# Optimization experiments

Measured on AMD Instinct MI355X. Metric: run time of the kernel, lower is better.

Reference implementation:

```python
import jax, jax.numpy as jnp
import numpy as np

NOISE_STD = 0.05
ALPHA = 0.2
RHO = 1.0
B, T, I, H, O = 128, 1000, 4, 512, 2

def setup_inputs() -> dict:
    key = jax.random.key(0)
    k_in, k_no, k_wi, k_wr, k_wo = jax.random.split(key, 5)
    return {
        "input": jax.random.normal(k_in, (B, T, I), dtype=jnp.float32),
        "noise": jax.random.normal(k_no, (B, T, H), dtype=jnp.float32),
        "wi": jax.random.normal(k_wi, (I, H), dtype=jnp.float32),
        "si": jnp.ones((I,), dtype=jnp.float32),
        "wrec": jax.random.normal(k_wr, (H, H), dtype=jnp.float32) * (RHO / np.sqrt(H)),
        "wo": jax.random.normal(k_wo, (H, O), dtype=jnp.float32) * (1.0 / np.sqrt(H)),
        "so": jnp.ones((O,), dtype=jnp.float32),
        "h0": jnp.zeros((H,), dtype=jnp.float32),
    }

def reference(input, noise, wi, si, wrec, wo, so, h0):
    # wi_full = (wi.T * si).T == wi * si[:, None]; wo_full = wo * so
    wi_full = wi * si[:, None]            # [I, H]
    wo_full = wo * so                     # [H, O]
    # pre-project inputs for all timesteps in one GEMM: [B, T, H]
    inp_proj = jnp.einsum('bti,ih->bth', input, wi_full)
    drive = NOISE_STD * noise + ALPHA * inp_proj  # fused per-step additive term
    h_init = jnp.broadcast_to(h0, (B, H))

    def step(h, d_t):
        r = jnp.tanh(h)
        h_new = h + d_t + ALPHA * (-h + r @ wrec.T)
        r_new = jnp.tanh(h_new)
        return h_new, r_new @ wo_full

    # scan over time: drive transposed to [T, B, H]
    _, out = jax.lax.scan(step, h_init, jnp.swapaxes(drive, 0, 1))
    return jnp.swapaxes(out, 0, 1)        # [B, T, O]
```

## Files before the change

### kernel.cpp

```cpp
#include <hip/hip_runtime.h>
#include <math.h>


#define Bn 128
#define Tn 1000
#define In 4
#define Hn 512
#define On 2
#define ALPHA 0.2f
#define NSTD 0.05f

#define KC 72
#define KR 128
#define KS (Hn - KC - KR)

__global__ void prep_kernel(const float* __restrict__ wi, const float* __restrict__ si,
                            const float* __restrict__ wrec, const float* __restrict__ wo,
                            const float* __restrict__ so,
                            float* __restrict__ wrecT, float* __restrict__ wi_full,
                            float* __restrict__ wo_full) {
    int idx = blockIdx.x * blockDim.x + threadIdx.x;
    int stride = gridDim.x * blockDim.x;
    for (int e = idx; e < Hn * Hn; e += stride) {
        int j = e & (Hn - 1);
        int k = e >> 9;
        wrecT[k * Hn + j] = wrec[j * Hn + k];
    }
    if (idx < In * Hn) wi_full[idx] = wi[idx] * si[idx >> 9];
    if (idx < Hn * On) wo_full[idx] = wo[idx] * so[idx & 1];
}

__global__ __launch_bounds__(512) void rnn_kernel(
    const float* __restrict__ input, const float* __restrict__ noise,
    const float* __restrict__ h0, const float* __restrict__ wrecT,
    const float* __restrict__ wi_full, const float* __restrict__ wo_full,
    float* __restrict__ out) {
    extern __shared__ float lds[];
    float* wlds = lds;
    float* r_s  = lds + KC * Hn;
    float* red  = r_s + Hn;

    const int j = threadIdx.x;
    const int b = blockIdx.x;

    for (int k = 0; k < KC; ++k)
        wlds[k * Hn + j] = wrecT[k * Hn + j];

    float wreg[KR];
#pragma unroll
    for (int k = 0; k < KR; ++k)
        wreg[k] = wrecT[(KC + k) * Hn + j];

    const float wi0 = wi_full[j],          wi1 = wi_full[Hn + j],
                wi2 = wi_full[2 * Hn + j], wi3 = wi_full[3 * Hn + j];
    const float wo0 = wo_full[j * On], wo1 = wo_full[j * On + 1];

    float h = h0[j];
    r_s[j] = tanhf(h);
    __syncthreads();

    const float* __restrict__ noise_p = noise + (size_t)b * Tn * Hn + j;
    const float* __restrict__ inp_p   = input + (size_t)b * Tn * In;
    float*       __restrict__ out_p   = out   + (size_t)b * Tn * On;
    const float* __restrict__ wstr    = wrecT + (size_t)(KC + KR) * Hn + j;

    const int lane = j & 63;
    const int wid  = j >> 6;
    const float4* r4 = (const float4*)r_s;

    for (int t = 0; t < Tn; ++t) {
        float  nz  = noise_p[(size_t)t * Hn];
        float4 inp = *(const float4*)(inp_p + t * In);

        float a0 = 0.f, a1 = 0.f, a2 = 0.f, a3 = 0.f;

#pragma unroll 6
        for (int g = 0; g < KC / 4; ++g) {
            float4 rv = r4[g];
            const float* wp = wlds + 4 * g * Hn + j;
            a0 = fmaf(rv.x, wp[0],      a0);
            a1 = fmaf(rv.y, wp[Hn],     a1);
            a2 = fmaf(rv.z, wp[2 * Hn], a2);
            a3 = fmaf(rv.w, wp[3 * Hn], a3);
        }
#pragma unroll
        for (int g = 0; g < KR / 4; ++g) {
            float4 rv = r4[KC / 4 + g];
            a0 = fmaf(rv.x, wreg[4 * g + 0], a0);
            a1 = fmaf(rv.y, wreg[4 * g + 1], a1);
            a2 = fmaf(rv.z, wreg[4 * g + 2], a2);
            a3 = fmaf(rv.w, wreg[4 * g + 3], a3);
        }
#pragma unroll 4
        for (int g = 0; g < KS / 4; ++g) {
            float4 rv = r4[(KC + KR) / 4 + g];
            const float* wp = wstr + (size_t)4 * g * Hn;
            a0 = fmaf(rv.x, wp[0],      a0);
            a1 = fmaf(rv.y, wp[Hn],     a1);
            a2 = fmaf(rv.z, wp[2 * Hn], a2);
            a3 = fmaf(rv.w, wp[3 * Hn], a3);
        }
        float acc = (a0 + a1) + (a2 + a3);

        float drive = NSTD * nz +
                      ALPHA * (inp.x * wi0 + inp.y * wi1 + inp.z * wi2 + inp.w * wi3);
        h = h + drive + ALPHA * (acc - h);
        float rn = tanhf(h);

        float p0 = rn * wo0, p1 = rn * wo1;
#pragma unroll
        for (int off = 32; off > 0; off >>= 1) {
            p0 += __shfl_down(p0, off, 64);
            p1 += __shfl_down(p1, off, 64);
        }

        __syncthreads();
        r_s[j] = rn;
        if (lane == 0) { red[wid * 2] = p0; red[wid * 2 + 1] = p1; }
        __syncthreads();
        if (j == 0) {
            float s0 = 0.f, s1 = 0.f;
#pragma unroll
            for (int w = 0; w < 8; ++w) { s0 += red[2 * w]; s1 += red[2 * w + 1]; }
            out_p[t * On]     = s0;
            out_p[t * On + 1] = s1;
        }
    }
}

extern "C" void kernel_launch(void* const* d_in, const int* in_sizes, int n_in,
                              void* d_out, int out_size, void* d_ws, size_t ws_size,
                              hipStream_t stream) {
    const float* input = (const float*)d_in[0];
    const float* noise = (const float*)d_in[1];
    const float* wi    = (const float*)d_in[2];
    const float* si    = (const float*)d_in[3];
    const float* wrec  = (const float*)d_in[4];
    const float* wo    = (const float*)d_in[5];
    const float* so    = (const float*)d_in[6];
    const float* h0    = (const float*)d_in[7];
    float* out = (float*)d_out;

    float* wrecT   = (float*)d_ws;
    float* wi_full = wrecT + Hn * Hn;
    float* wo_full = wi_full + In * Hn;

    prep_kernel<<<512, 512, 0, stream>>>(wi, si, wrec, wo, so, wrecT, wi_full, wo_full);

    const size_t lds_bytes = (size_t)(KC * Hn + Hn + 16) * sizeof(float);
    hipFuncSetAttribute((const void*)rnn_kernel,
                        hipFuncAttributeMaxDynamicSharedMemorySize, (int)lds_bytes);
    rnn_kernel<<<Bn, Hn, lds_bytes, stream>>>(input, noise, h0, wrecT, wi_full,
                                              wo_full, out);
}
```

Baseline: 9.673 ms.

## Split each batch row across two workgroups exchanging hidden state via global flags

Each batch element is now handled by two 512-thread workgroups, each owning half of the hidden units. Within a workgroup the two 256-thread halves split the K dimension. The halves of a pair trade their new tanh activations each step through a double-buffered global buffer with acquire/release flag spinning, and add output partial sums atomically. This puts the whole recurrent weight matrix in LDS and registers rather than streaming part of it from global memory, and doubles the number of CUs in use. The cost is a cross-workgroup spin-wait every timestep, which relies on both workgroups of a pair being resident at once and adds latency on the serial critical path.

```diff
diff --git a/kernel.cpp b/kernel.cpp
--- a/kernel.cpp
+++ b/kernel.cpp
@@ -10,15 +10,16 @@
 #define ALPHA 0.2f
 #define NSTD 0.05f
 
-#define KC 72
-#define KR 128
-#define KS (Hn - KC - KR)
+#define HALF 256
+#define LR 72
+#define RR 92
 
 __global__ void prep_kernel(const float* __restrict__ wi, const float* __restrict__ si,
                             const float* __restrict__ wrec, const float* __restrict__ wo,
                             const float* __restrict__ so,
                             float* __restrict__ wrecT, float* __restrict__ wi_full,
-                            float* __restrict__ wo_full) {
+                            float* __restrict__ wo_full, float* __restrict__ out,
+                            int* __restrict__ flags) {
     int idx = blockIdx.x * blockDim.x + threadIdx.x;
     int stride = gridDim.x * blockDim.x;
     for (int e = idx; e < Hn * Hn; e += stride) {
@@ -28,102 +29,171 @@
     }
     if (idx < In * Hn) wi_full[idx] = wi[idx] * si[idx >> 9];
     if (idx < Hn * On) wo_full[idx] = wo[idx] * so[idx & 1];
+    for (int e = idx; e < Bn * Tn * On; e += stride) out[e] = 0.f;
+    if (idx < Bn * 2) flags[idx] = 0;
 }
 
-__global__ __launch_bounds__(512) void rnn_kernel(
+__global__ __launch_bounds__(512, 2) void rnn_kernel(
     const float* __restrict__ input, const float* __restrict__ noise,
     const float* __restrict__ h0, const float* __restrict__ wrecT,
     const float* __restrict__ wi_full, const float* __restrict__ wo_full,
-    float* __restrict__ out) {
+    float* xbuf, int* flags, float* __restrict__ out) {
     extern __shared__ float lds[];
-    float* wlds = lds;
-    float* r_s  = lds + KC * Hn;
-    float* red  = r_s + Hn;
-
-    const int j = threadIdx.x;
-    const int b = blockIdx.x;
-
-    for (int k = 0; k < KC; ++k)
-        wlds[k * Hn + j] = wrecT[k * Hn + j];
-
-    float wreg[KR];
-#pragma unroll
-    for (int k = 0; k < KR; ++k)
-        wreg[k] = wrecT[(KC + k) * Hn + j];
-
-    const float wi0 = wi_full[j],          wi1 = wi_full[Hn + j],
-                wi2 = wi_full[2 * Hn + j], wi3 = wi_full[3 * Hn + j];
-    const float wo0 = wo_full[j * On], wo1 = wo_full[j * On + 1];
-
-    float h = h0[j];
-    r_s[j] = tanhf(h);
+    float* wl0  = lds;
+    float* wl1  = lds + LR * HALF;
+    float* r_s  = lds + 2 * LR * HALF;
+    float* pacc = r_s + Hn;
+    float* red  = pacc + HALF;
+
+    const int tid  = threadIdx.x;
+    const int c    = tid & (HALF - 1);
+    const int hh   = tid >> 8;
+
+    const int bid  = blockIdx.x;
+    const int g    = bid & 7;
+    const int s    = bid >> 3;
+    const int b    = g * 16 + (s >> 1);
+    const int half = s & 1;
+
+    const int base0 = half * HALF;
+    const int base1 = (1 - half) * HALF;
+    const int gc    = half * HALF + c;
+
+    for (int e = tid; e < LR * HALF; e += 512) {
+        int lr = e >> 8;
+        int cc = e & 255;
+        int dst = (lr >> 2) * 1024 + cc * 4 + (lr & 3);
+        wl0[dst] = wrecT[(base0 + lr) * Hn + half * HALF + cc];
+        wl1[dst] = wrecT[(base1 + lr) * Hn + half * HALF + cc];
+    }
+
+    float w0[RR], w1[RR];
+#pragma unroll
+    for (int i = 0; i < RR; ++i)
+        w0[i] = wrecT[(base0 + LR + hh * RR + i) * Hn + gc];
+#pragma unroll
+    for (int i = 0; i < RR; ++i)
+        w1[i] = wrecT[(base1 + LR + hh * RR + i) * Hn + gc];
+#pragma unroll
+    for (int i = 0; i < RR; ++i) asm volatile("" : "+v"(w0[i]));
+#pragma unroll
+    for (int i = 0; i < RR; ++i) asm volatile("" : "+v"(w1[i]));
+
+    const float wi0 = wi_full[0 * Hn + gc], wi1 = wi_full[1 * Hn + gc],
+                wi2 = wi_full[2 * Hn + gc], wi3 = wi_full[3 * Hn + gc];
+    const float wo0 = wo_full[gc * On + 0], wo1 = wo_full[gc * On + 1];
+
+    float h = h0[gc];
+    r_s[tid] = tanhf(h0[tid]);
     __syncthreads();
 
-    const float* __restrict__ noise_p = noise + (size_t)b * Tn * Hn + j;
-    const float* __restrict__ inp_p   = input + (size_t)b * Tn * In;
-    float*       __restrict__ out_p   = out   + (size_t)b * Tn * On;
-    const float* __restrict__ wstr    = wrecT + (size_t)(KC + KR) * Hn + j;
-
-    const int lane = j & 63;
-    const int wid  = j >> 6;
-    const float4* r4 = (const float4*)r_s;
+    const float* noise_p = noise + (size_t)b * Tn * Hn + half * HALF + c;
+    const float* inp_p   = input + (size_t)b * Tn * In;
+    float*       out_p   = out   + (size_t)b * Tn * On;
+
+    float*       xb_mine = xbuf + (size_t)((b * 2 + half) * 2) * HALF;
+    const float* xb_part = xbuf + (size_t)((b * 2 + (1 - half)) * 2) * HALF;
+    int* flag_mine    = flags + b * 2 + half;
+    int* flag_partner = flags + b * 2 + (1 - half);
+
+    const float4* r4    = (const float4*)r_s;
+    const float4* wl4_0 = (const float4*)wl0;
+    const float4* wl4_1 = (const float4*)wl1;
+    const int rB0 = base0 >> 2, rB1 = base1 >> 2;
 
     for (int t = 0; t < Tn; ++t) {
-        float  nz  = noise_p[(size_t)t * Hn];
-        float4 inp = *(const float4*)(inp_p + t * In);
+        float nz = 0.f;
+        float4 inp = {0.f, 0.f, 0.f, 0.f};
+        if (hh == 0) {
+            nz  = noise_p[(size_t)t * Hn];
+            inp = *(const float4*)(inp_p + t * In);
+        }
 
         float a0 = 0.f, a1 = 0.f, a2 = 0.f, a3 = 0.f;
 
-#pragma unroll 6
-        for (int g = 0; g < KC / 4; ++g) {
-            float4 rv = r4[g];
-            const float* wp = wlds + 4 * g * Hn + j;
-            a0 = fmaf(rv.x, wp[0],      a0);
-            a1 = fmaf(rv.y, wp[Hn],     a1);
-            a2 = fmaf(rv.z, wp[2 * Hn], a2);
-            a3 = fmaf(rv.w, wp[3 * Hn], a3);
-        }
-#pragma unroll
-        for (int g = 0; g < KR / 4; ++g) {
-            float4 rv = r4[KC / 4 + g];
-            a0 = fmaf(rv.x, wreg[4 * g + 0], a0);
-            a1 = fmaf(rv.y, wreg[4 * g + 1], a1);
-            a2 = fmaf(rv.z, wreg[4 * g + 2], a2);
-            a3 = fmaf(rv.w, wreg[4 * g + 3], a3);
-        }
-#pragma unroll 4
-        for (int g = 0; g < KS / 4; ++g) {
-            float4 rv = r4[(KC + KR) / 4 + g];
-            const float* wp = wstr + (size_t)4 * g * Hn;
-            a0 = fmaf(rv.x, wp[0],      a0);
-            a1 = fmaf(rv.y, wp[Hn],     a1);
-            a2 = fmaf(rv.z, wp[2 * Hn], a2);
-            a3 = fmaf(rv.w, wp[3 * Hn], a3);
-        }
+#pragma unroll
+        for (int m = 0; m < LR / 8; ++m) {
+            float4 wv = wl4_0[(hh * 9 + m) * 256 + c];
+            float4 rv = r4[rB0 + hh * 9 + m];
+            a0 = fmaf(rv.x, wv.x, a0);
+            a1 = fmaf(rv.y, wv.y, a1);
+            a2 = fmaf(rv.z, wv.z, a2);
+            a3 = fmaf(rv.w, wv.w, a3);
+        }
+#pragma unroll
+        for (int m = 0; m < RR / 4; ++m) {
+            float4 rv = r4[rB0 + (LR >> 2) + hh * (RR >> 2) + m];
+            a0 = fmaf(rv.x, w0[4 * m + 0], a0);
+            a1 = fmaf(rv.y, w0[4 * m + 1], a1);
+            a2 = fmaf(rv.z, w0[4 * m + 2], a2);
+            a3 = fmaf(rv.w, w0[4 * m + 3], a3);
+        }
+
+        if (t > 0) {
+            if (tid == 0) {
+                while (__hip_atomic_load(flag_partner, __ATOMIC_ACQUIRE,
+                                         __HIP_MEMORY_SCOPE_AGENT) < t) {
+                    __builtin_amdgcn_s_sleep(1);
+                }
+            }
+            __syncthreads();
+            if (tid < HALF)
+                r_s[base1 + tid] = __hip_atomic_load(
+                    &xb_part[(t & 1) * HALF + tid], __ATOMIC_RELAXED,
+                    __HIP_MEMORY_SCOPE_AGENT);
+            __syncthreads();
+        }
+
+#pragma unroll
+        for (int m = 0; m < LR / 8; ++m) {
+            float4 wv = wl4_1[(hh * 9 + m) * 256 + c];
+            float4 rv = r4[rB1 + hh * 9 + m];
+            a0 = fmaf(rv.x, wv.x, a0);
+            a1 = fmaf(rv.y, wv.y, a1);
+            a2 = fmaf(rv.z, wv.z, a2);
+            a3 = fmaf(rv.w, wv.w, a3);
+        }
+#pragma unroll
+        for (int m = 0; m < RR / 4; ++m) {
+            float4 rv = r4[rB1 + (LR >> 2) + hh * (RR >> 2) + m];
+            a0 = fmaf(rv.x, w1[4 * m + 0], a0);
+            a1 = fmaf(rv.y, w1[4 * m + 1], a1);
+            a2 = fmaf(rv.z, w1[4 * m + 2], a2);
+            a3 = fmaf(rv.w, w1[4 * m + 3], a3);
+        }
+
         float acc = (a0 + a1) + (a2 + a3);
-
-        float drive = NSTD * nz +
-                      ALPHA * (inp.x * wi0 + inp.y * wi1 + inp.z * wi2 + inp.w * wi3);
-        h = h + drive + ALPHA * (acc - h);
-        float rn = tanhf(h);
-
-        float p0 = rn * wo0, p1 = rn * wo1;
-#pragma unroll
-        for (int off = 32; off > 0; off >>= 1) {
-            p0 += __shfl_down(p0, off, 64);
-            p1 += __shfl_down(p1, off, 64);
-        }
-
+        if (hh == 1) pacc[c] = acc;
         __syncthreads();
-        r_s[j] = rn;
-        if (lane == 0) { red[wid * 2] = p0; red[wid * 2 + 1] = p1; }
+        if (hh == 0) {
+            float total = acc + pacc[c];
+            float drive = NSTD * nz +
+                          ALPHA * (inp.x * wi0 + inp.y * wi1 +
+                                   inp.z * wi2 + inp.w * wi3);
+            h = h + drive + ALPHA * (total - h);
+            float rn = tanhf(h);
+            r_s[base0 + c] = rn;
+            xb_mine[((t + 1) & 1) * HALF + c] = rn;
+            float p0 = rn * wo0, p1 = rn * wo1;
+#pragma unroll
+            for (int off = 32; off > 0; off >>= 1) {
+                p0 += __shfl_down(p0, off, 64);
+                p1 += __shfl_down(p1, off, 64);
+            }
+            if ((tid & 63) == 0) {
+                red[(tid >> 6) * 2 + 0] = p0;
+                red[(tid >> 6) * 2 + 1] = p1;
+            }
+        }
         __syncthreads();
-        if (j == 0) {
-            float s0 = 0.f, s1 = 0.f;
-#pragma unroll
-            for (int w = 0; w < 8; ++w) { s0 += red[2 * w]; s1 += red[2 * w + 1]; }
-            out_p[t * On]     = s0;
-            out_p[t * On + 1] = s1;
+        if (tid == 0) {
+            __threadfence();
+            __hip_atomic_store(flag_mine, t + 1, __ATOMIC_RELEASE,
+                               __HIP_MEMORY_SCOPE_AGENT);
+            float s0 = red[0] + red[2] + red[4] + red[6];
+            float s1 = red[1] + red[3] + red[5] + red[7];
+            atomicAdd(&out_p[t * On + 0], s0);
+            atomicAdd(&out_p[t * On + 1], s1);
         }
     }
 }
@@ -144,12 +214,17 @@
     float* wrecT   = (float*)d_ws;
     float* wi_full = wrecT + Hn * Hn;
     float* wo_full = wi_full + In * Hn;
-
-    prep_kernel<<<512, 512, 0, stream>>>(wi, si, wrec, wo, so, wrecT, wi_full, wo_full);
-
-    const size_t lds_bytes = (size_t)(KC * Hn + Hn + 16) * sizeof(float);
+    float* xbuf    = wo_full + Hn * On;
+    int*   flags   = (int*)(xbuf + Bn * 2 * 2 * HALF);
+
+    prep_kernel<<<512, 512, 0, stream>>>(wi, si, wrec, wo, so, wrecT, wi_full,
+                                         wo_full, out, flags);
+
+    const size_t lds_bytes =
+        (size_t)(2 * LR * HALF + Hn + HALF + 8) * sizeof(float);
     hipFuncSetAttribute((const void*)rnn_kernel,
                         hipFuncAttributeMaxDynamicSharedMemorySize, (int)lds_bytes);
-    rnn_kernel<<<Bn, Hn, lds_bytes, stream>>>(input, noise, h0, wrecT, wi_full,
-                                              wo_full, out);
+    rnn_kernel<<<2 * Bn, 512, lds_bytes, stream>>>(input, noise, h0, wrecT,
+                                                   wi_full, wo_full, xbuf, flags,
+                                                   out);
 }
```

New measurement: 36.02 ms. 3.72x slower.
